# Kernel optimization log

Hardware: AMD Instinct MI355X
Metric: run time of the kernel (lower is better)

## Reference

```python
import jax, jax.numpy as jnp
import numpy as np

NH = 8          # n_heads
CLIP = 10.0     # tanh_clipping


def _make_heads(x):
    # (B, n, H) -> (B, NH, n, H//NH)
    B, n, H = x.shape
    return x.reshape(B, n, NH, H // NH).transpose(0, 2, 1, 3)


def setup_inputs() -> dict:
    key = jax.random.key(0)
    ks = jax.random.split(key, 12)
    B, N, G, H = 64, 2000, 128, 128
    s = 1.0 / np.sqrt(H)
    embeddings = jax.random.normal(ks[0], (B, N, H), jnp.float32)
    u = jax.random.uniform(ks[1], (B, G, N))
    group_ninf_mask = jnp.where(u < 0.1, -1e9, 0.0).astype(jnp.float32)
    w = lambda k: (jax.random.normal(k, (H, H), jnp.float32) * s)
    return {
        'embeddings': embeddings,
        'group_ninf_mask': group_ninf_mask,
        'Wq_graph': w(ks[2]), 'Wq_source': w(ks[3]), 'Wq_target': w(ks[4]),
        'Wq_last': w(ks[5]), 'Wk': w(ks[6]), 'Wv': w(ks[7]),
        'Wc': w(ks[8]), 'bc': jnp.zeros((H,), jnp.float32),
        'source_node': jax.random.randint(ks[9], (B,), 0, N),
        'target_node': jax.random.randint(ks[10], (B,), 0, N),
        'last_node': jax.random.randint(ks[11], (B, G), 0, N),
    }


def reference(embeddings, group_ninf_mask, Wq_graph, Wq_source, Wq_target,
              Wq_last, Wk, Wv, Wc, bc, source_node, target_node, last_node):
    B, N, H = embeddings.shape
    G = group_ninf_mask.shape[1]
    hd = H // NH
    b = jnp.arange(B)

    # --- reset() state ---
    graph_emb = embeddings.mean(axis=1, keepdims=True)              # (B,1,H)
    q_graph = _make_heads(graph_emb @ Wq_graph.T)                   # (B,NH,1,hd)
    src_emb = embeddings[b, source_node][:, None, :]                # (B,1,H)
    q_source = _make_heads(src_emb @ Wq_source.T)
    tgt_emb = embeddings[b, target_node][:, None, :]                # (B,1,H)
    q_target = _make_heads(tgt_emb @ Wq_target.T)
    glimpse_k = _make_heads(embeddings @ Wk.T)                      # (B,NH,N,hd)
    glimpse_v = _make_heads(embeddings @ Wv.T)                      # (B,NH,N,hd)

    # --- forward(last_node) ---
    last_emb = embeddings[b[:, None], last_node]                    # (B,G,H)
    q_last = _make_heads(last_emb @ Wq_last.T)                      # (B,NH,G,hd)
    glimpse_q = q_graph + q_source + q_target + q_last              # (B,NH,G,hd)

    scores = jnp.einsum('bhgd,bhnd->bhgn', glimpse_q, glimpse_k) / np.sqrt(hd)
    scores = scores + group_ninf_mask[:, None, :, :]                # mask per head
    attn = jax.nn.softmax(scores, axis=-1)                          # (B,NH,G,N)
    heads = jnp.einsum('bhgn,bhnd->bhgd', attn, glimpse_v)          # (B,NH,G,hd)
    mh_out = heads.transpose(0, 2, 1, 3).reshape(B, G, H)           # (B,G,H)
    final_q = mh_out @ Wc.T + bc                                    # multi_head_combine

    # single-head logits vs logit_k = embeddings^T, tanh-clipped + masked
    logits = jnp.einsum('bgh,bnh->bgn', final_q, embeddings) / np.sqrt(H)
    logits = CLIP * jnp.tanh(logits) + group_ninf_mask
    probs = jax.nn.softmax(logits, axis=2)                          # (B,G,N)
    return probs
```

## Files before the change

### kernel.cpp

```cpp
#include <hip/hip_runtime.h>
#include <hip/hip_bf16.h>

#define BB 64
#define NN 2000
#define GG 128
#define HH 128
#define NHEAD 8
#define HD 16

typedef __attribute__((ext_vector_type(8))) short short8;
typedef __attribute__((ext_vector_type(4))) float f32x4;

__device__ __forceinline__ unsigned short bf16hi(float f) {
    union { float f; unsigned u; } v; v.f = f;
    return (unsigned short)(v.u >> 16);
}
__device__ __forceinline__ float bf16tof(unsigned short h) {
    union { float f; unsigned u; } v; v.u = ((unsigned)h) << 16;
    return v.f;
}

__device__ __forceinline__ void cvt8(const float4& v0, const float4& v1,
                                     short8& hi, short8& lo) {
    float fv[8] = {v0.x, v0.y, v0.z, v0.w, v1.x, v1.y, v1.z, v1.w};
#pragma unroll
    for (int i = 0; i < 8; ++i) {
        unsigned short h = bf16hi(fv[i]);
        hi[i] = (short)h;
        lo[i] = (short)bf16hi(fv[i] - bf16tof(h));
    }
}

__device__ __forceinline__ void fma8x8(const float4& a0, const float4& a1,
                                       const float4& b0, const float4& b1,
                                       float acc[8][8]) {
    const float av[8] = {a0.x, a0.y, a0.z, a0.w, a1.x, a1.y, a1.z, a1.w};
    const float bv[8] = {b0.x, b0.y, b0.z, b0.w, b1.x, b1.y, b1.z, b1.w};
#pragma unroll
    for (int i = 0; i < 8; ++i)
#pragma unroll
        for (int k = 0; k < 8; ++k) acc[i][k] += av[i] * bv[k];
}

__global__ __launch_bounds__(256) void k_wt(const float* w0, const float* w1, const float* w2,
                     const float* w3, const float* w4, const float* w5,
                     const float* w6, float* WT,
                     unsigned short* Wkhi, unsigned short* Wklo,
                     unsigned short* Wvhi, unsigned short* Wvlo) {
    int m = blockIdx.x;
    if (m >= 5) {
        const float* src = (m == 5) ? w4 : w5;
        unsigned short* dh = (m == 5) ? Wkhi : Wvhi;
        unsigned short* dl = (m == 5) ? Wklo : Wvlo;
        for (int e = threadIdx.x * 4; e < 16384; e += 1024) {
            float4 v = *(const float4*)(src + e);
            float fv[4] = {v.x, v.y, v.z, v.w};
            unsigned short h4[4], l4[4];
#pragma unroll
            for (int i = 0; i < 4; ++i) {
                h4[i] = bf16hi(fv[i]); l4[i] = bf16hi(fv[i] - bf16tof(h4[i]));
            }
            uint2 ph, pl;
            ph.x = h4[0] | (h4[1] << 16); ph.y = h4[2] | (h4[3] << 16);
            pl.x = l4[0] | (l4[1] << 16); pl.y = l4[2] | (l4[3] << 16);
            *(uint2*)(dh + e) = ph;
            *(uint2*)(dl + e) = pl;
        }
        return;
    }
    __shared__ float t[128 * 129];
    const float* src = (m == 0) ? w0 : (m == 1) ? w1 : (m == 2) ? w2 : (m == 3) ? w3 : w6;
    int slot = (m == 4) ? 6 : m;
    for (int e = threadIdx.x; e < 16384; e += 256) {
        int c = e >> 7, j = e & 127;
        t[c * 129 + j] = src[e];
    }
    __syncthreads();
    for (int e = threadIdx.x; e < 16384; e += 256) {
        int j = e >> 7, c = e & 127;
        WT[slot * 16384 + e] = t[c * 129 + j];
    }
}

__global__ __launch_bounds__(256) void k_maskbits(const float* mask, unsigned long long* bits) {
    int bg = blockIdx.x;
    int lane = threadIdx.x & 63;
    int wv = threadIdx.x >> 6;
    for (int w = wv; w < 32; w += 4) {
        int n = w * 64 + lane;
        bool keep = false;
        if (n < NN) keep = (mask[(size_t)bg * NN + n] == 0.0f);
        unsigned long long bal = __ballot(keep);
        if (lane == 0) bits[bg * 32 + w] = bal;
    }
}

__global__ __launch_bounds__(128) void k_gsum(const float* emb, float* gpart) {
    int ck = blockIdx.x, b = blockIdx.y, c = threadIdx.x;
    const float* p = emb + ((size_t)b * NN + ck * 125) * HH + c;
    float s = 0.0f;
#pragma unroll 5
    for (int r = 0; r < 125; ++r) s += p[(size_t)r * HH];
    gpart[ck * 8192 + b * 128 + c] = s;
}

__global__ __launch_bounds__(128) void k_qbase(const float* emb, const int* srcn, const int* tgtn,
                        const float* gpart, const float* WT, float* qbase) {
    int b = blockIdx.x, c = threadIdx.x;
    __shared__ float ge[128], se[128], te[128];
    float s = 0.0f;
#pragma unroll
    for (int t = 0; t < 16; ++t) s += gpart[t * 8192 + b * 128 + c];
    ge[c] = s * (1.0f / 2000.0f);
    se[c] = emb[((size_t)b * NN + srcn[b]) * HH + c];
    te[c] = emb[((size_t)b * NN + tgtn[b]) * HH + c];
    __syncthreads();
    const float* Wg = WT;
    const float* Ws = WT + 16384;
    const float* Wt2 = WT + 32768;
    float acc = 0.0f;
#pragma unroll 4
    for (int j = 0; j < 128; ++j) {
        acc += ge[j] * Wg[j * 128 + c] + se[j] * Ws[j * 128 + c] + te[j] * Wt2[j * 128 + c];
    }
    qbase[b * 128 + c] = acc;
}

__global__ __launch_bounds__(256) void k_qlast(const float* emb, const int* lastn, const float* WT,
                        const float* qbase, unsigned short* Qhi, unsigned short* Qlo) {
    int b = blockIdx.x;
    int tid = threadIdx.x, xq = tid & 15, yq = tid >> 4;
    __shared__ float Bl[128 * 132];
    for (int e = tid; e < 16384; e += 256) {
        int g = e >> 7, j = e & 127;
        Bl[j * 132 + g] = emb[((size_t)b * NN + lastn[b * 128 + g]) * HH + j];
    }
    __syncthreads();
    const float* Wql = WT + 3 * 16384;
    float acc[8][8] = {};
#pragma unroll 4
    for (int j = 0; j < 128; ++j) {
        const float4* Ar = (const float4*)(Wql + j * 128);
        float4 a0 = Ar[yq], a1 = Ar[16 + yq];
        const float4* Br = (const float4*)(Bl + j * 132);
        float4 b0 = Br[xq], b1 = Br[16 + xq];
        fma8x8(a0, a1, b0, b1, acc);
    }
    float4 qb0 = *(const float4*)(qbase + b * 128 + 4 * yq);
    float4 qb1 = *(const float4*)(qbase + b * 128 + 64 + 4 * yq);
    const float q0v[4] = {qb0.x, qb0.y, qb0.z, qb0.w};
    const float q1v[4] = {qb1.x, qb1.y, qb1.z, qb1.w};
#pragma unroll
    for (int k = 0; k < 8; ++k) {
        int g = (k < 4) ? (4 * xq + k) : (64 + 4 * xq + (k - 4));
        size_t base = ((size_t)b * 128 + g) * 128;
        unsigned short h4[4], l4[4];
#pragma unroll
        for (int i = 0; i < 4; ++i) {
            float f = (acc[i][k] + q0v[i]) * 0.25f;
            h4[i] = bf16hi(f); l4[i] = bf16hi(f - bf16tof(h4[i]));
        }
        uint2 ph, pl;
        ph.x = h4[0] | (h4[1] << 16); ph.y = h4[2] | (h4[3] << 16);
        pl.x = l4[0] | (l4[1] << 16); pl.y = l4[2] | (l4[3] << 16);
        *(uint2*)(Qhi + base + 4 * yq) = ph;
        *(uint2*)(Qlo + base + 4 * yq) = pl;
#pragma unroll
        for (int i = 0; i < 4; ++i) {
            float f = (acc[4 + i][k] + q1v[i]) * 0.25f;
            h4[i] = bf16hi(f); l4[i] = bf16hi(f - bf16tof(h4[i]));
        }
        ph.x = h4[0] | (h4[1] << 16); ph.y = h4[2] | (h4[3] << 16);
        pl.x = l4[0] | (l4[1] << 16); pl.y = l4[2] | (l4[3] << 16);
        *(uint2*)(Qhi + base + 64 + 4 * yq) = ph;
        *(uint2*)(Qlo + base + 64 + 4 * yq) = pl;
    }
}

__global__ __launch_bounds__(256, 4) void k_kv(const float* emb,
        const unsigned short* Wkhi, const unsigned short* Wklo,
        const unsigned short* Wvhi, const unsigned short* Wvlo,
        unsigned short* Khi, unsigned short* Klo,
        unsigned short* Vhi, unsigned short* Vlo) {
    int nt = blockIdx.x, b = blockIdx.y;
    int tid = threadIdx.x;
    int wv = tid >> 6, lane = tid & 63, l15 = lane & 15, q3 = lane >> 4;
    int n0 = nt * 128;

    short8 eh[2][4], el[2][4];
#pragma unroll
    for (int t = 0; t < 2; ++t) {
        int n = n0 + wv * 32 + t * 16 + l15;
        const float* rowp = emb + ((size_t)b * NN + n) * HH + q3 * 8;
        bool ok = (n < NN);
#pragma unroll
        for (int ks = 0; ks < 4; ++ks) {
            float4 v0 = make_float4(0.f, 0.f, 0.f, 0.f), v1 = v0;
            if (ok) {
                v0 = *(const float4*)(rowp + ks * 32);
                v1 = *(const float4*)(rowp + ks * 32 + 4);
            }
            cvt8(v0, v1, eh[t][ks], el[t][ks]);
        }
    }

#pragma unroll
    for (int ct = 0; ct < 8; ++ct) {
        f32x4 aK[2] = {{0.f, 0.f, 0.f, 0.f}, {0.f, 0.f, 0.f, 0.f}};
        f32x4 aV[2] = {{0.f, 0.f, 0.f, 0.f}, {0.f, 0.f, 0.f, 0.f}};
#pragma unroll
        for (int ks = 0; ks < 4; ++ks) {
            size_t woff = ((size_t)(ct * 16 + l15)) * 128 + ks * 32 + q3 * 8;
            short8 wkh = *(const short8*)(Wkhi + woff);
            short8 wkl = *(const short8*)(Wklo + woff);
            short8 wvh = *(const short8*)(Wvhi + woff);
            short8 wvl = *(const short8*)(Wvlo + woff);
#pragma unroll
            for (int t = 0; t < 2; ++t) {
                aK[t] = __builtin_amdgcn_mfma_f32_16x16x32_bf16(wkh, eh[t][ks], aK[t], 0, 0, 0);
                aK[t] = __builtin_amdgcn_mfma_f32_16x16x32_bf16(wkh, el[t][ks], aK[t], 0, 0, 0);
                aK[t] = __builtin_amdgcn_mfma_f32_16x16x32_bf16(wkl, eh[t][ks], aK[t], 0, 0, 0);
                aV[t] = __builtin_amdgcn_mfma_f32_16x16x32_bf16(eh[t][ks], wvh, aV[t], 0, 0, 0);
                aV[t] = __builtin_amdgcn_mfma_f32_16x16x32_bf16(el[t][ks], wvh, aV[t], 0, 0, 0);
                aV[t] = __builtin_amdgcn_mfma_f32_16x16x32_bf16(eh[t][ks], wvl, aV[t], 0, 0, 0);
            }
        }
#pragma unroll
        for (int t = 0; t < 2; ++t) {
            int kn = n0 + wv * 32 + t * 16 + l15;
            if (kn < NN) {
                unsigned short h4[4], l4[4];
#pragma unroll
                for (int r = 0; r < 4; ++r) {
                    float f = aK[t][r];
                    h4[r] = bf16hi(f); l4[r] = bf16hi(f - bf16tof(h4[r]));
                }
                uint2 ph, pl;
                ph.x = h4[0] | (h4[1] << 16); ph.y = h4[2] | (h4[3] << 16);
                pl.x = l4[0] | (l4[1] << 16); pl.y = l4[2] | (l4[3] << 16);
                size_t kbase = (((size_t)b * 8 + ct) * 2000 + kn) * 16 + 4 * q3;
                *(uint2*)(Khi + kbase) = ph;
                *(uint2*)(Klo + kbase) = pl;
            }
            int nb = n0 + wv * 32 + t * 16 + 4 * q3;
            if (nb + 3 < NN) {
                unsigned short h4[4], l4[4];
#pragma unroll
                for (int r = 0; r < 4; ++r) {
                    float f = aV[t][r];
                    h4[r] = bf16hi(f); l4[r] = bf16hi(f - bf16tof(h4[r]));
                }
                uint2 ph, pl;
                ph.x = h4[0] | (h4[1] << 16); ph.y = h4[2] | (h4[3] << 16);
                pl.x = l4[0] | (l4[1] << 16); pl.y = l4[2] | (l4[3] << 16);
                size_t vbase = (((size_t)b * 8 + ct) * 16 + l15) * 2000 + nb;
                *(uint2*)(Vhi + vbase) = ph;
                *(uint2*)(Vlo + vbase) = pl;
            }
        }
    }
}

__global__ __launch_bounds__(256) void k_flash(const unsigned short* Khi, const unsigned short* Klo,
                        const unsigned short* Vhi, const unsigned short* Vlo,
                        const unsigned short* Qhi, const unsigned short* Qlo,
                        const unsigned long long* bits, float* Opart, float* Zpart) {
    int bid = blockIdx.x;
    int s4 = bid & 3, h = (bid >> 2) & 7, b = bid >> 5;
    int tid = threadIdx.x;
    int wv = tid >> 6, lane = tid & 63, l15 = lane & 15, q3 = lane >> 4;

    __shared__ unsigned short Klds[2][64][24];
    __shared__ unsigned short Vlds[2][16][72];
    __shared__ unsigned short Plds[4][2][32][72];

    const short8 z8 = {0, 0, 0, 0, 0, 0, 0, 0};

    short8 qf[2][2];
#pragma unroll
    for (int gt = 0; gt < 2; ++gt) {
        int g = wv * 32 + gt * 16 + l15;
        if (q3 < 2) {
            size_t off = ((size_t)b * 128 + g) * 128 + h * 16 + q3 * 8;
            qf[gt][0] = *(const short8*)(Qhi + off);
            qf[gt][1] = *(const short8*)(Qlo + off);
        } else {
            qf[gt][0] = z8; qf[gt][1] = z8;
        }
    }

    f32x4 Oacc[2] = {{0.f, 0.f, 0.f, 0.f}, {0.f, 0.f, 0.f, 0.f}};
    float zacc[2] = {0.f, 0.f};

    const unsigned long long* bb0 = bits + (((size_t)b * 128 + wv * 32 + l15) * 32);
    const unsigned long long* bb1 = bb0 + 16 * 32;

    size_t kvbase = ((size_t)b * 8 + h);
    const unsigned short* Kh = Khi + kvbase * 2000 * 16;
    const unsigned short* Kl = Klo + kvbase * 2000 * 16;
    const unsigned short* Vh = Vhi + kvbase * 16 * 2000;
    const unsigned short* Vl = Vlo + kvbase * 16 * 2000;

    int snr = tid >> 2, sj4 = (tid & 3) * 4;
    int svd = tid >> 4, svn = (tid & 15) * 4;

    for (int ch = s4 * 8; ch < s4 * 8 + 8; ++ch) {
        int n0 = ch * 64;
        __syncthreads();
        {
            uint2 zz; zz.x = 0; zz.y = 0;
            int n = n0 + snr;
            uint2 k0 = zz, k1 = zz;
            if (n < NN) {
                size_t off = ((size_t)n) * 16 + sj4;
                k0 = *(const uint2*)(Kh + off);
                k1 = *(const uint2*)(Kl + off);
            }
            *(uint2*)&Klds[0][snr][sj4] = k0;
            *(uint2*)&Klds[1][snr][sj4] = k1;
            int vn = n0 + svn;
            uint2 v0 = zz, v1 = zz;
            if (vn + 3 < NN) {
                size_t off = ((size_t)svd) * 2000 + vn;
                v0 = *(const uint2*)(Vh + off);
                v1 = *(const uint2*)(Vl + off);
            }
            *(uint2*)&Vlds[0][svd][svn] = v0;
            *(uint2*)&Vlds[1][svd][svn] = v1;
        }
        __syncthreads();

        unsigned long long wm0 = bb0[ch];
        unsigned long long wm1 = bb1[ch];

        f32x4 S[4][2];
#pragma unroll
        for (int nt = 0; nt < 4; ++nt) {
            short8 kh, kl;
            if (q3 < 2) {
                kh = *(const short8*)&Klds[0][nt * 16 + l15][q3 * 8];
                kl = *(const short8*)&Klds[1][nt * 16 + l15][q3 * 8];
            } else { kh = z8; kl = z8; }
#pragma unroll
            for (int gt = 0; gt < 2; ++gt) {
                f32x4 c = {0.f, 0.f, 0.f, 0.f};
                c = __builtin_amdgcn_mfma_f32_16x16x32_bf16(kh, qf[gt][0], c, 0, 0, 0);
                c = __builtin_amdgcn_mfma_f32_16x16x32_bf16(kh, qf[gt][1], c, 0, 0, 0);
                c = __builtin_amdgcn_mfma_f32_16x16x32_bf16(kl, qf[gt][0], c, 0, 0, 0);
                S[nt][gt] = c;
            }
        }

#pragma unroll
        for (int nt = 0; nt < 4; ++nt) {
#pragma unroll
            for (int gt = 0; gt < 2; ++gt) {
                unsigned long long wm = gt ? wm1 : wm0;
                float p[4];
#pragma unroll
                for (int r = 0; r < 4; ++r) {
                    int sh = nt * 16 + q3 * 4 + r;
                    float e = ((wm >> sh) & 1ull) ? __expf(S[nt][gt][r]) : 0.0f;
                    p[r] = e;
                    zacc[gt] += e;
                }
                unsigned short h4[4], l4[4];
#pragma unroll
                for (int r = 0; r < 4; ++r) {
                    h4[r] = bf16hi(p[r]); l4[r] = bf16hi(p[r] - bf16tof(h4[r]));
                }
                uint2 ph, pl;
                ph.x = h4[0] | (h4[1] << 16); ph.y = h4[2] | (h4[3] << 16);
                pl.x = l4[0] | (l4[1] << 16); pl.y = l4[2] | (l4[3] << 16);
                *(uint2*)&Plds[wv][0][gt * 16 + l15][nt * 16 + q3 * 4] = ph;
                *(uint2*)&Plds[wv][1][gt * 16 + l15][nt * 16 + q3 * 4] = pl;
            }
        }

#pragma unroll
        for (int ks = 0; ks < 2; ++ks) {
            short8 vh = *(const short8*)&Vlds[0][l15][ks * 32 + q3 * 8];
            short8 vl = *(const short8*)&Vlds[1][l15][ks * 32 + q3 * 8];
#pragma unroll
            for (int gt = 0; gt < 2; ++gt) {
                short8 ph = *(const short8*)&Plds[wv][0][gt * 16 + l15][ks * 32 + q3 * 8];
                short8 pl = *(const short8*)&Plds[wv][1][gt * 16 + l15][ks * 32 + q3 * 8];
                Oacc[gt] = __builtin_amdgcn_mfma_f32_16x16x32_bf16(vh, ph, Oacc[gt], 0, 0, 0);
                Oacc[gt] = __builtin_amdgcn_mfma_f32_16x16x32_bf16(vh, pl, Oacc[gt], 0, 0, 0);
                Oacc[gt] = __builtin_amdgcn_mfma_f32_16x16x32_bf16(vl, ph, Oacc[gt], 0, 0, 0);
            }
        }
    }

    size_t obase = (((size_t)s4 * 64 + b) * 8 + h);
#pragma unroll
    for (int gt = 0; gt < 2; ++gt) {
        float z = zacc[gt];
        z += __shfl_xor(z, 16);
        z += __shfl_xor(z, 32);
        int g = wv * 32 + gt * 16 + l15;
        if (q3 == 0) Zpart[obase * 128 + g] = z;
#pragma unroll
        for (int r = 0; r < 4; ++r) {
            int d = q3 * 4 + r;
            Opart[(obase * 16 + d) * 128 + g] = Oacc[gt][r];
        }
    }
}

__global__ __launch_bounds__(256) void k_ocomb(const float* Opart, const float* Zpart, float* MHt) {
    int bh = blockIdx.x;
    int b = bh >> 3, h = bh & 7;
    int tid = threadIdx.x;
    for (int e = tid; e < 2048; e += 256) {
        int d = e >> 7, g = e & 127;
        float z = 0.0f, o = 0.0f;
#pragma unroll
        for (int s = 0; s < 4; ++s) {
            z += Zpart[(((size_t)s * 64 + b) * 8 + h) * 128 + g];
            o += Opart[((((size_t)s * 64 + b) * 8 + h) * 16 + d) * 128 + g];
        }
        MHt[((size_t)b * 128 + h * 16 + d) * 128 + g] = o / z;
    }
}

__global__ __launch_bounds__(256) void k_fq(const float* MHt, const float* WT, const float* bcv,
                                            unsigned short* FQhi, unsigned short* FQlo) {
    int b = blockIdx.x;
    int tid = threadIdx.x, xq = tid & 15, yq = tid >> 4;
    __shared__ float Bl[128 * 132];
    for (int e = tid; e < 16384; e += 256) {
        int j = e >> 7, g = e & 127;
        Bl[j * 132 + g] = MHt[(size_t)b * 16384 + e];
    }
    __syncthreads();
    const float* Wc = WT + 6 * 16384;
    float acc[8][8] = {};
#pragma unroll 4
    for (int j = 0; j < 128; ++j) {
        const float4* Ar = (const float4*)(Wc + j * 128);
        float4 a0 = Ar[yq], a1 = Ar[16 + yq];
        const float4* Br = (const float4*)(Bl + j * 132);
        float4 b0 = Br[xq], b1 = Br[16 + xq];
        fma8x8(a0, a1, b0, b1, acc);
    }
    float4 bc0 = *(const float4*)(bcv + 4 * yq);
    float4 bc1 = *(const float4*)(bcv + 64 + 4 * yq);
    const float bcv8[8] = {bc0.x, bc0.y, bc0.z, bc0.w, bc1.x, bc1.y, bc1.z, bc1.w};
    const float sc = 0.08838834764831845f;
#pragma unroll
    for (int k = 0; k < 8; ++k) {
        int g = (k < 4) ? (4 * xq + k) : (64 + 4 * xq + (k - 4));
        size_t base = ((size_t)b * 128 + g) * 128;
        unsigned short h4[4], l4[4];
#pragma unroll
        for (int i = 0; i < 4; ++i) {
            float f = (acc[i][k] + bcv8[i]) * sc;
            h4[i] = bf16hi(f); l4[i] = bf16hi(f - bf16tof(h4[i]));
        }
        uint2 ph, pl;
        ph.x = h4[0] | (h4[1] << 16); ph.y = h4[2] | (h4[3] << 16);
        pl.x = l4[0] | (l4[1] << 16); pl.y = l4[2] | (l4[3] << 16);
        *(uint2*)(FQhi + base + 4 * yq) = ph;
        *(uint2*)(FQlo + base + 4 * yq) = pl;
#pragma unroll
        for (int i = 0; i < 4; ++i) {
            float f = (acc[4 + i][k] + bcv8[4 + i]) * sc;
            h4[i] = bf16hi(f); l4[i] = bf16hi(f - bf16tof(h4[i]));
        }
        ph.x = h4[0] | (h4[1] << 16); ph.y = h4[2] | (h4[3] << 16);
        pl.x = l4[0] | (l4[1] << 16); pl.y = l4[2] | (l4[3] << 16);
        *(uint2*)(FQhi + base + 64 + 4 * yq) = ph;
        *(uint2*)(FQlo + base + 64 + 4 * yq) = pl;
    }
}

__global__ __launch_bounds__(256, 4) void k_logits(const float* emb,
        const unsigned short* FQhi, const unsigned short* FQlo,
        const unsigned long long* bits, float* out, float* Zp) {
    int nt = blockIdx.x, b = blockIdx.y;
    int tid = threadIdx.x;
    int wv = tid >> 6, lane = tid & 63, l15 = lane & 15, q3 = lane >> 4;
    int n0 = nt * 128;

    short8 beh[2][4], bel[2][4];
#pragma unroll
    for (int t = 0; t < 2; ++t) {
        int n = n0 + wv * 32 + t * 16 + l15;
        const float* rowp = emb + ((size_t)b * NN + n) * HH + q3 * 8;
        bool ok = (n < NN);
#pragma unroll
        for (int ks = 0; ks < 4; ++ks) {
            float4 v0 = make_float4(0.f, 0.f, 0.f, 0.f), v1 = v0;
            if (ok) {
                v0 = *(const float4*)(rowp + ks * 32);
                v1 = *(const float4*)(rowp + ks * 32 + 4);
            }
            cvt8(v0, v1, beh[t][ks], bel[t][ks]);
        }
    }

    const unsigned long long* bb = bits + (size_t)b * 128 * 32;
    int g = 0;
#pragma unroll
    for (int gt = 0; gt < 8; ++gt) {
        f32x4 acc[2] = {{0.f, 0.f, 0.f, 0.f}, {0.f, 0.f, 0.f, 0.f}};
#pragma unroll
        for (int ks = 0; ks < 4; ++ks) {
            size_t foff = ((size_t)b * 128 + gt * 16 + l15) * 128 + ks * 32 + q3 * 8;
            short8 fh = *(const short8*)(FQhi + foff);
            short8 fl = *(const short8*)(FQlo + foff);
#pragma unroll
            for (int t = 0; t < 2; ++t) {
                acc[t] = __builtin_amdgcn_mfma_f32_16x16x32_bf16(beh[t][ks], fh, acc[t], 0, 0, 0);
                acc[t] = __builtin_amdgcn_mfma_f32_16x16x32_bf16(bel[t][ks], fh, acc[t], 0, 0, 0);
                acc[t] = __builtin_amdgcn_mfma_f32_16x16x32_bf16(beh[t][ks], fl, acc[t], 0, 0, 0);
            }
        }
        g = gt * 16 + l15;
        float psum = 0.f;
#pragma unroll
        for (int t = 0; t < 2; ++t) {
            int nb = n0 + wv * 32 + t * 16 + 4 * q3;
            int word = (n0 + wv * 32 + t * 16) >> 6;
            unsigned long long wm = bb[g * 32 + word];
            float pv[4];
#pragma unroll
            for (int r = 0; r < 4; ++r) {
                int n = nb + r;
                float l = acc[t][r];
                float e2 = __expf(2.0f * l);
                float th = 1.0f - 2.0f / (e2 + 1.0f);
                float p = ((wm >> (n & 63)) & 1ull) ? __expf(10.0f * th) : 0.0f;
                pv[r] = p;
                psum += p;
            }
            if (nb + 3 < NN) {
                *(float4*)(out + ((size_t)b * 128 + g) * NN + nb) =
                    make_float4(pv[0], pv[1], pv[2], pv[3]);
            }
        }
        psum += __shfl_xor(psum, 16);
        psum += __shfl_xor(psum, 32);
        if (q3 == 0) Zp[((size_t)(nt * 4 + wv)) * 8192 + b * 128 + g] = psum;
    }
}

__global__ __launch_bounds__(256) void k_norm(const float* Zp, float* out) {
    int bg = blockIdx.x;
    __shared__ float invs;
    if (threadIdx.x == 0) {
        float s = 0.0f;
#pragma unroll
        for (int t = 0; t < 64; ++t) s += Zp[(size_t)t * 8192 + bg];
        invs = 1.0f / s;
    }
    __syncthreads();
    float inv = invs;
    for (int n = threadIdx.x; n < NN; n += 256) out[(size_t)bg * NN + n] *= inv;
}

extern "C" void kernel_launch(void* const* d_in, const int* in_sizes, int n_in,
                              void* d_out, int out_size, void* d_ws, size_t ws_size,
                              hipStream_t stream) {
    const float* emb = (const float*)d_in[0];
    const float* mask = (const float*)d_in[1];
    const float* Wqg = (const float*)d_in[2];
    const float* Wqs = (const float*)d_in[3];
    const float* Wqt = (const float*)d_in[4];
    const float* Wql = (const float*)d_in[5];
    const float* Wk = (const float*)d_in[6];
    const float* Wv = (const float*)d_in[7];
    const float* Wc = (const float*)d_in[8];
    const float* bc = (const float*)d_in[9];
    const int* srcn = (const int*)d_in[10];
    const int* tgtn = (const int*)d_in[11];
    const int* lastn = (const int*)d_in[12];
    float* out = (float*)d_out;

    float* ws = (float*)d_ws;
    float* WT = ws;
    unsigned short* Wkhi = (unsigned short*)(WT + 4 * 16384);
    unsigned short* Wklo = Wkhi + 16384;
    unsigned short* Wvhi = Wklo + 16384;
    unsigned short* Wvlo = Wvhi + 16384;
    float* gpart = ws + 114688;
    float* qbase = ws + 245760;
    float* MHt = ws + 253952;
    unsigned short* FQhi = (unsigned short*)(ws + 1302528);
    unsigned short* FQlo = FQhi + 1048576;
    float* Zp = ws + 2351104;
    unsigned short* Khi = (unsigned short*)(ws + 3399680);
    unsigned short* Klo = (unsigned short*)(ws + 11591680);
    unsigned short* Vhi = (unsigned short*)(ws + 19783680);
    unsigned short* Vlo = (unsigned short*)(ws + 27975680);
    unsigned long long* bits = (unsigned long long*)(ws + 36167680);

    float* Opart = out;
    float* Zpart = out + 4194304;
    unsigned short* Qhi = (unsigned short*)(out + 4456448);
    unsigned short* Qlo = Qhi + 1048576;

    k_wt<<<7, 256, 0, stream>>>(Wqg, Wqs, Wqt, Wql, Wk, Wv, Wc, WT, Wkhi, Wklo, Wvhi, Wvlo);
    k_maskbits<<<8192, 256, 0, stream>>>(mask, bits);
    k_gsum<<<dim3(16, 64), 128, 0, stream>>>(emb, gpart);
    k_kv<<<dim3(16, 64), 256, 0, stream>>>(emb, Wkhi, Wklo, Wvhi, Wvlo, Khi, Klo, Vhi, Vlo);
    k_qbase<<<64, 128, 0, stream>>>(emb, srcn, tgtn, gpart, WT, qbase);
    k_qlast<<<64, 256, 0, stream>>>(emb, lastn, WT, qbase, Qhi, Qlo);
    k_flash<<<2048, 256, 0, stream>>>(Khi, Klo, Vhi, Vlo, Qhi, Qlo, bits, Opart, Zpart);
    k_ocomb<<<512, 256, 0, stream>>>(Opart, Zpart, MHt);
    k_fq<<<64, 256, 0, stream>>>(MHt, WT, bc, FQhi, FQlo);
    k_logits<<<dim3(16, 64), 256, 0, stream>>>(emb, FQhi, FQlo, bits, out, Zp);
    k_norm<<<8192, 256, 0, stream>>>(Zp, out);
}
```

Baseline: 361.0 us.

## Drop LDS staging in flash kernel; load K/V directly and shuffle P in registers

The flash-attention kernel no longer stages K and V tiles through shared memory with two block barriers per chunk. Each lane now loads its MFMA operands straight from global memory, and the P tile is rebuilt for the PV MFMA layout with cross-lane shuffles instead of an LDS round trip. Launch bounds now request 4 waves per SIMD to raise occupancy. This removes the barriers and LDS traffic, at the cost of redundant global loads across waves, many shuffle instructions, and possible register pressure.

After: 677.5 us. 87.7% more time.

```diff
diff --git a/kernel.cpp b/kernel.cpp
--- a/kernel.cpp
+++ b/kernel.cpp
@@ -261,7 +261,7 @@
     }
 }
 
-__global__ __launch_bounds__(256) void k_flash(const unsigned short* Khi, const unsigned short* Klo,
+__global__ __launch_bounds__(256, 4) void k_flash(const unsigned short* Khi, const unsigned short* Klo,
                         const unsigned short* Vhi, const unsigned short* Vlo,
                         const unsigned short* Qhi, const unsigned short* Qlo,
                         const unsigned long long* bits, float* Opart, float* Zpart) {
@@ -269,10 +269,6 @@
     int s4 = bid & 3, h = (bid >> 2) & 7, b = bid >> 5;
     int tid = threadIdx.x;
     int wv = tid >> 6, lane = tid & 63, l15 = lane & 15, q3 = lane >> 4;
-
-    __shared__ unsigned short Klds[2][64][24];
-    __shared__ unsigned short Vlds[2][16][72];
-    __shared__ unsigned short Plds[4][2][32][72];
 
     const short8 z8 = {0, 0, 0, 0, 0, 0, 0, 0};
 
@@ -296,71 +292,42 @@
     const unsigned long long* bb1 = bb0 + 16 * 32;
 
     size_t kvbase = ((size_t)b * 8 + h);
-    const unsigned short* Kh = Khi + kvbase * 2000 * 16;
-    const unsigned short* Kl = Klo + kvbase * 2000 * 16;
-    const unsigned short* Vh = Vhi + kvbase * 16 * 2000;
-    const unsigned short* Vl = Vlo + kvbase * 16 * 2000;
-
-    int snr = tid >> 2, sj4 = (tid & 3) * 4;
-    int svd = tid >> 4, svn = (tid & 15) * 4;
+    const unsigned short* Kh = Khi + kvbase * 32000;
+    const unsigned short* Kl = Klo + kvbase * 32000;
+    const unsigned short* Vh = Vhi + kvbase * 32000;
+    const unsigned short* Vl = Vlo + kvbase * 32000;
+
+    int laneA = ((q3 & 1) << 5) + l15;
+    int laneB = laneA + 16;
+    bool hiSel = (q3 & 2) != 0;
 
     for (int ch = s4 * 8; ch < s4 * 8 + 8; ++ch) {
         int n0 = ch * 64;
-        __syncthreads();
-        {
-            uint2 zz; zz.x = 0; zz.y = 0;
-            int n = n0 + snr;
-            uint2 k0 = zz, k1 = zz;
-            if (n < NN) {
-                size_t off = ((size_t)n) * 16 + sj4;
-                k0 = *(const uint2*)(Kh + off);
-                k1 = *(const uint2*)(Kl + off);
-            }
-            *(uint2*)&Klds[0][snr][sj4] = k0;
-            *(uint2*)&Klds[1][snr][sj4] = k1;
-            int vn = n0 + svn;
-            uint2 v0 = zz, v1 = zz;
-            if (vn + 3 < NN) {
-                size_t off = ((size_t)svd) * 2000 + vn;
-                v0 = *(const uint2*)(Vh + off);
-                v1 = *(const uint2*)(Vl + off);
-            }
-            *(uint2*)&Vlds[0][svd][svn] = v0;
-            *(uint2*)&Vlds[1][svd][svn] = v1;
-        }
-        __syncthreads();
-
         unsigned long long wm0 = bb0[ch];
         unsigned long long wm1 = bb1[ch];
 
-        f32x4 S[4][2];
+        unsigned hi0[4][2], hi1[4][2], lo0[4][2], lo1[4][2];
 #pragma unroll
         for (int nt = 0; nt < 4; ++nt) {
-            short8 kh, kl;
-            if (q3 < 2) {
-                kh = *(const short8*)&Klds[0][nt * 16 + l15][q3 * 8];
-                kl = *(const short8*)&Klds[1][nt * 16 + l15][q3 * 8];
-            } else { kh = z8; kl = z8; }
+            short8 kh = z8, kl = z8;
+            int kn = n0 + nt * 16 + l15;
+            if (q3 < 2 && kn < NN) {
+                size_t koff = ((size_t)kn) * 16 + q3 * 8;
+                kh = *(const short8*)(Kh + koff);
+                kl = *(const short8*)(Kl + koff);
+            }
 #pragma unroll
             for (int gt = 0; gt < 2; ++gt) {
                 f32x4 c = {0.f, 0.f, 0.f, 0.f};
                 c = __builtin_amdgcn_mfma_f32_16x16x32_bf16(kh, qf[gt][0], c, 0, 0, 0);
                 c = __builtin_amdgcn_mfma_f32_16x16x32_bf16(kh, qf[gt][1], c, 0, 0, 0);
                 c = __builtin_amdgcn_mfma_f32_16x16x32_bf16(kl, qf[gt][0], c, 0, 0, 0);
-                S[nt][gt] = c;
-            }
-        }
-
-#pragma unroll
-        for (int nt = 0; nt < 4; ++nt) {
-#pragma unroll
-            for (int gt = 0; gt < 2; ++gt) {
                 unsigned long long wm = gt ? wm1 : wm0;
                 float p[4];
 #pragma unroll
                 for (int r = 0; r < 4; ++r) {
                     int sh = nt * 16 + q3 * 4 + r;
-                    float e = ((wm >> sh) & 1ull) ? __expf(S[nt][gt][r]) : 0.0f;
+                    float e = ((wm >> sh) & 1ull) ? __expf(c[r]) : 0.0f;
                     p[r] = e;
                     zacc[gt] += e;
                 }
@@ -369,22 +336,47 @@
                 for (int r = 0; r < 4; ++r) {
                     h4[r] = bf16hi(p[r]); l4[r] = bf16hi(p[r] - bf16tof(h4[r]));
                 }
-                uint2 ph, pl;
-                ph.x = h4[0] | (h4[1] << 16); ph.y = h4[2] | (h4[3] << 16);
-                pl.x = l4[0] | (l4[1] << 16); pl.y = l4[2] | (l4[3] << 16);
-                *(uint2*)&Plds[wv][0][gt * 16 + l15][nt * 16 + q3 * 4] = ph;
-                *(uint2*)&Plds[wv][1][gt * 16 + l15][nt * 16 + q3 * 4] = pl;
+                hi0[nt][gt] = (unsigned)h4[0] | ((unsigned)h4[1] << 16);
+                hi1[nt][gt] = (unsigned)h4[2] | ((unsigned)h4[3] << 16);
+                lo0[nt][gt] = (unsigned)l4[0] | ((unsigned)l4[1] << 16);
+                lo1[nt][gt] = (unsigned)l4[2] | ((unsigned)l4[3] << 16);
             }
         }
 
 #pragma unroll
         for (int ks = 0; ks < 2; ++ks) {
-            short8 vh = *(const short8*)&Vlds[0][l15][ks * 32 + q3 * 8];
-            short8 vl = *(const short8*)&Vlds[1][l15][ks * 32 + q3 * 8];
+            short8 vh = z8, vl = z8;
+            int vn = n0 + ks * 32 + q3 * 8;
+            if (vn < NN) {
+                size_t voff = (size_t)l15 * 2000 + vn;
+                vh = *(const short8*)(Vh + voff);
+                vl = *(const short8*)(Vl + voff);
+            }
+            int nta = 2 * ks, ntb = 2 * ks + 1;
 #pragma unroll
             for (int gt = 0; gt < 2; ++gt) {
-                short8 ph = *(const short8*)&Plds[wv][0][gt * 16 + l15][ks * 32 + q3 * 8];
-                short8 pl = *(const short8*)&Plds[wv][1][gt * 16 + l15][ks * 32 + q3 * 8];
+                uint4 hw, lw;
+                {
+                    unsigned a, bsh;
+                    a = __shfl(hi0[nta][gt], laneA); bsh = __shfl(hi0[ntb][gt], laneA);
+                    hw.x = hiSel ? bsh : a;
+                    a = __shfl(hi1[nta][gt], laneA); bsh = __shfl(hi1[ntb][gt], laneA);
+                    hw.y = hiSel ? bsh : a;
+                    a = __shfl(hi0[nta][gt], laneB); bsh = __shfl(hi0[ntb][gt], laneB);
+                    hw.z = hiSel ? bsh : a;
+                    a = __shfl(hi1[nta][gt], laneB); bsh = __shfl(hi1[ntb][gt], laneB);
+                    hw.w = hiSel ? bsh : a;
+                    a = __shfl(lo0[nta][gt], laneA); bsh = __shfl(lo0[ntb][gt], laneA);
+                    lw.x = hiSel ? bsh : a;
+                    a = __shfl(lo1[nta][gt], laneA); bsh = __shfl(lo1[ntb][gt], laneA);
+                    lw.y = hiSel ? bsh : a;
+                    a = __shfl(lo0[nta][gt], laneB); bsh = __shfl(lo0[ntb][gt], laneB);
+                    lw.z = hiSel ? bsh : a;
+                    a = __shfl(lo1[nta][gt], laneB); bsh = __shfl(lo1[ntb][gt], laneB);
+                    lw.w = hiSel ? bsh : a;
+                }
+                short8 ph = *(short8*)&hw;
+                short8 pl = *(short8*)&lw;
                 Oacc[gt] = __builtin_amdgcn_mfma_f32_16x16x32_bf16(vh, ph, Oacc[gt], 0, 0, 0);
                 Oacc[gt] = __builtin_amdgcn_mfma_f32_16x16x32_bf16(vh, pl, Oacc[gt], 0, 0, 0);
                 Oacc[gt] = __builtin_amdgcn_mfma_f32_16x16x32_bf16(vl, ph, Oacc[gt], 0, 0, 0);
```
